# Optimization experiments

Hardware: AMD Instinct MI355X
Metric: run time of the kernel (lower is better)

Reference implementation:

```python
import jax, jax.numpy as jnp
import numpy as np
import math

B, T, D, SLOTS, TOPK = 8, 4096, 512, 128, 8


def setup_inputs() -> dict:
    key = jax.random.key(0)
    kq, kK, kV = jax.random.split(key, 3)
    # xavier_uniform for [slots, d_model]: bound = sqrt(6/(slots+d_model))
    bound = math.sqrt(6.0 / (SLOTS + D))
    return {
        "q": jax.random.normal(kq, (B, T, D), dtype=jnp.float32),
        "K": jax.random.uniform(kK, (SLOTS, D), minval=-bound, maxval=bound, dtype=jnp.float32),
        "V": jax.random.uniform(kV, (SLOTS, D), minval=-bound, maxval=bound, dtype=jnp.float32),
        "salience": jnp.zeros((SLOTS,), dtype=jnp.float32),
        "topk": TOPK,
    }


def reference(q, K, V, salience, topk):
    # q: [B,T,D], K/V: [S,D], salience: [S]
    Bq, Tq, Dq = q.shape
    k = min(topk, K.shape[0])
    scores = jnp.einsum('btd,sd->bts', q, K) / jnp.sqrt(jnp.float32(Dq))
    scores = scores + salience[None, None, :]
    topk_scores, topk_indices = jax.lax.top_k(scores, k)          # [B,T,k]
    attention_weights = jax.nn.softmax(topk_scores, axis=-1)      # [B,T,k]
    V_selected = V[topk_indices]                                  # [B,T,k,D] gather
    read_vectors = jnp.einsum('btk,btkd->btd', attention_weights, V_selected)
    return read_vectors, attention_weights
```

## Files before the change

kernel.cpp:

```cpp
#include <hip/hip_runtime.h>
#include <hip/hip_bf16.h>
#include <math.h>

#define R_TOTAL 32768
#define DM      512
#define NSLOT   128
#define KSEL    8

typedef _Float16 half8 __attribute__((ext_vector_type(8)));
typedef float    floatx4 __attribute__((ext_vector_type(4)));

__global__ void smb_prepK(const float* __restrict__ Km, _Float16* __restrict__ Ks) {
  const int i = blockIdx.x * 256 + threadIdx.x;
  const int slot = i >> 9;
  const int d    = i & 511;
  const float f  = Km[i] * 256.0f;
  const _Float16 h  = (_Float16)f;
  const _Float16 lo = (_Float16)(f - (float)h);
  const int c  = d >> 5;
  const int kg = (d >> 3) & 3;
  const int j  = d & 7;
  Ks[((((c * 8) + kg    ) * NSLOT + slot) << 3) + j] = h;
  Ks[((((c * 8) + 4 + kg) * NSLOT + slot) << 3) + j] = lo;
}

__device__ __forceinline__ void load16_lds(const _Float16* g, _Float16* l) {
  __builtin_amdgcn_global_load_lds(
      (const __attribute__((address_space(1))) unsigned int*)g,
      (__attribute__((address_space(3))) unsigned int*)l, 16, 0, 0);
}

__global__ __launch_bounds__(512, 8) void smb_main(
    const float* __restrict__ q,
    const _Float16* __restrict__ Ks,
    const float* __restrict__ Vm,
    const float* __restrict__ sal,
    float* __restrict__ outv,
    float* __restrict__ outw)
{
  __shared__ union U {
    _Float16 stage[2][8][NSLOT][8];
    float    slab[64][132];
  } u;

  const int t  = threadIdx.x;
  const int w  = t >> 6;
  const int l  = t & 63;
  const int li = l & 15;
  const int kg = l >> 4;
  const int rg = w >> 1;
  const int sh = w & 1;
  const int r0b = blockIdx.x * 64;
  const int r0w = r0b + rg * 16;

  const float* qrow = q + (size_t)(r0w + li) * DM + kg * 8;

  floatx4 acc[4];
#pragma unroll
  for (int g = 0; g < 4; ++g) acc[g] = (floatx4){0.f, 0.f, 0.f, 0.f};

#pragma unroll
  for (int p = 0; p < 2; ++p) {
    const _Float16* src = Ks + ((((size_t)0 * 8 + w) * NSLOT + p * 64 + l) << 3);
    load16_lds(src, &u.stage[0][w][p * 64 + l][0]);
  }
  float4 q0c = *(const float4*)(qrow + 0);
  float4 q1c = *(const float4*)(qrow + 4);
  float4 q0n = *(const float4*)(qrow + 32);
  float4 q1n = *(const float4*)(qrow + 36);
  __syncthreads();

#pragma unroll 2
  for (int c = 0; c < 16; ++c) {
    const int cb = c & 1, nb = cb ^ 1;
    float4 q0nn, q1nn;
    if (c < 15) {
#pragma unroll
      for (int p = 0; p < 2; ++p) {
        const _Float16* src = Ks + ((((size_t)(c + 1) * 8 + w) * NSLOT + p * 64 + l) << 3);
        load16_lds(src, &u.stage[nb][w][p * 64 + l][0]);
      }
    }
    if (c < 14) {
      q0nn = *(const float4*)(qrow + (c + 2) * 32);
      q1nn = *(const float4*)(qrow + (c + 2) * 32 + 4);
    }

    half8 a1, a2;
#pragma unroll
    for (int j = 0; j < 4; ++j) {
      const float f0 = q0c[j] * 16.0f;
      const float f1 = q1c[j] * 16.0f;
      const _Float16 h0 = (_Float16)f0;
      const _Float16 h1 = (_Float16)f1;
      a1[j]     = h0;  a2[j]     = (_Float16)(f0 - (float)h0);
      a1[4 + j] = h1;  a2[4 + j] = (_Float16)(f1 - (float)h1);
    }
#pragma unroll
    for (int g = 0; g < 4; ++g) {
      const int slot = sh * 64 + g * 16 + li;
      const half8 b1 = *(const half8*)&u.stage[cb][kg][slot][0];
      const half8 b2 = *(const half8*)&u.stage[cb][4 + kg][slot][0];
      acc[g] = __builtin_amdgcn_mfma_f32_16x16x32_f16(a1, b1, acc[g], 0, 0, 0);
      acc[g] = __builtin_amdgcn_mfma_f32_16x16x32_f16(a2, b1, acc[g], 0, 0, 0);
      acc[g] = __builtin_amdgcn_mfma_f32_16x16x32_f16(a1, b2, acc[g], 0, 0, 0);
    }
    q0c = q0n; q1c = q1n;
    if (c < 14) { q0n = q0nn; q1n = q1nn; }
    __syncthreads();
  }

  const float den = sqrtf((float)DM);
#pragma unroll
  for (int g = 0; g < 4; ++g) {
    const int col = sh * 64 + g * 16 + li;
    const float sv = sal[col];
#pragma unroll
    for (int i = 0; i < 4; ++i) {
      const float s = (acc[g][i] * 0.000244140625f) / den + sv;
      u.slab[rg * 16 + kg * 4 + i][col] = s;
    }
  }
  __syncthreads();

  const int row = t >> 3;
  const int lq  = t & 7;

  float bs[8]; int bi[8];
#pragma unroll
  for (int p = 0; p < 8; ++p) { bs[p] = -3.0e38f; bi[p] = 0x7fffffff; }

#pragma unroll
  for (int jj = 0; jj < 16; ++jj) {
    const int   j = jj * 8 + lq;
    const float s = u.slab[row][j];
    bool c[8];
#pragma unroll
    for (int p = 0; p < 8; ++p) c[p] = s > bs[p];
    float nb[8]; int ni[8];
    nb[0] = c[0] ? s : bs[0];
    ni[0] = c[0] ? j : bi[0];
#pragma unroll
    for (int p = 7; p >= 1; --p) {
      nb[p] = c[p] ? (c[p - 1] ? bs[p - 1] : s) : bs[p];
      ni[p] = c[p] ? (c[p - 1] ? bi[p - 1] : j) : bi[p];
    }
#pragma unroll
    for (int p = 0; p < 8; ++p) { bs[p] = nb[p]; bi[p] = ni[p]; }
  }

  float ts[8]; int ti_[8];
#pragma unroll
  for (int r = 0; r < 8; ++r) {
    float hs = bs[0]; int hi = bi[0];
#pragma unroll
    for (int m = 1; m <= 4; m <<= 1) {
      const float os = __shfl_xor(hs, m, 64);
      const int   oi = __shfl_xor(hi, m, 64);
      if (os > hs || (os == hs && oi < hi)) { hs = os; hi = oi; }
    }
    ts[r] = hs; ti_[r] = hi;
    if (bs[0] == hs && bi[0] == hi) {
#pragma unroll
      for (int p = 0; p < 7; ++p) { bs[p] = bs[p + 1]; bi[p] = bi[p + 1]; }
      bs[7] = -3.0e38f; bi[7] = 0x7fffffff;
    }
  }

  float tw[8];
  const float mx = ts[0];
  float esum = 0.0f;
#pragma unroll
  for (int r = 0; r < 8; ++r) { tw[r] = expf(ts[r] - mx); esum += tw[r]; }
#pragma unroll
  for (int r = 0; r < 8; ++r) tw[r] /= esum;

  if (lq == 0) {
#pragma unroll
    for (int r = 0; r < 8; ++r) outw[(size_t)(r0b + row) * KSEL + r] = tw[r];
  }

  const float4* __restrict__ V4 = (const float4*)Vm;
  float4* __restrict__ O4 = (float4*)outv;
  const size_t obase = (size_t)(r0b + row) * (DM / 4);
#pragma unroll 4
  for (int cc = 0; cc < 16; ++cc) {
    const int cdx = cc * 8 + lq;
    float4 a; a.x = a.y = a.z = a.w = 0.0f;
#pragma unroll
    for (int r = 0; r < 8; ++r) {
      const float4 v = V4[(size_t)ti_[r] * (DM / 4) + cdx];
      a.x = fmaf(tw[r], v.x, a.x);
      a.y = fmaf(tw[r], v.y, a.y);
      a.z = fmaf(tw[r], v.z, a.z);
      a.w = fmaf(tw[r], v.w, a.w);
    }
    O4[obase + cdx] = a;
  }
}

extern "C" void kernel_launch(void* const* d_in, const int* in_sizes, int n_in,
                              void* d_out, int out_size, void* d_ws, size_t ws_size,
                              hipStream_t stream) {
  const float* q   = (const float*)d_in[0];
  const float* Km  = (const float*)d_in[1];
  const float* Vm  = (const float*)d_in[2];
  const float* sal = (const float*)d_in[3];

  float* outv = (float*)d_out;
  float* outw = outv + (size_t)R_TOTAL * DM;

  _Float16* Ks = (_Float16*)d_ws;

  hipLaunchKernelGGL(smb_prepK, dim3((NSLOT * DM) / 256), dim3(256), 0, stream, Km, Ks);
  hipLaunchKernelGGL(smb_main, dim3(R_TOTAL / 64), dim3(512), 0, stream,
                     q, Ks, Vm, sal, outv, outw);
}
```

Baseline: 68.59 us.

## Double K-chunk width per pipeline stage and vectorize top-k slab reads

The GEMM loop now processes two 32-wide K chunks per iteration (8 iterations instead of 16), staging twice as much of K in LDS per stage. This halves the number of barriers and prefetch rounds. The top-k scan now gives each thread a contiguous 16-element segment read with float4 LDS loads instead of strided scalar reads, and occupancy hint drops from 8 to 4 blocks per CU. The larger LDS stage (32KB union) may reduce occupancy.

After: 68.11 us. No clear change (-0.7%).

```diff
diff --git a/kernel.cpp b/kernel.cpp
--- a/kernel.cpp
+++ b/kernel.cpp
@@ -30,7 +30,7 @@
       (__attribute__((address_space(3))) unsigned int*)l, 16, 0, 0);
 }
 
-__global__ __launch_bounds__(512, 8) void smb_main(
+__global__ __launch_bounds__(512, 4) void smb_main(
     const float* __restrict__ q,
     const _Float16* __restrict__ Ks,
     const float* __restrict__ Vm,
@@ -39,7 +39,7 @@
     float* __restrict__ outw)
 {
   __shared__ union U {
-    _Float16 stage[2][8][NSLOT][8];
+    _Float16 stage[2][2][8][NSLOT][8];
     float    slab[64][132];
   } u;
 
@@ -60,53 +60,60 @@
   for (int g = 0; g < 4; ++g) acc[g] = (floatx4){0.f, 0.f, 0.f, 0.f};
 
 #pragma unroll
-  for (int p = 0; p < 2; ++p) {
-    const _Float16* src = Ks + ((((size_t)0 * 8 + w) * NSLOT + p * 64 + l) << 3);
-    load16_lds(src, &u.stage[0][w][p * 64 + l][0]);
-  }
-  float4 q0c = *(const float4*)(qrow + 0);
-  float4 q1c = *(const float4*)(qrow + 4);
-  float4 q0n = *(const float4*)(qrow + 32);
-  float4 q1n = *(const float4*)(qrow + 36);
+  for (int i = 0; i < 4; ++i) {
+    const int sub = i >> 1, p = i & 1;
+    const _Float16* src = Ks + ((((size_t)(0 + sub) * 8 + w) * NSLOT + p * 64 + l) << 3);
+    load16_lds(src, &u.stage[0][sub][w][p * 64 + l][0]);
+  }
+  float4 qc0 = *(const float4*)(qrow + 0);
+  float4 qc1 = *(const float4*)(qrow + 4);
+  float4 qc2 = *(const float4*)(qrow + 32);
+  float4 qc3 = *(const float4*)(qrow + 36);
   __syncthreads();
 
 #pragma unroll 2
-  for (int c = 0; c < 16; ++c) {
+  for (int c = 0; c < 8; ++c) {
     const int cb = c & 1, nb = cb ^ 1;
-    float4 q0nn, q1nn;
-    if (c < 15) {
-#pragma unroll
-      for (int p = 0; p < 2; ++p) {
-        const _Float16* src = Ks + ((((size_t)(c + 1) * 8 + w) * NSLOT + p * 64 + l) << 3);
-        load16_lds(src, &u.stage[nb][w][p * 64 + l][0]);
-      }
-    }
-    if (c < 14) {
-      q0nn = *(const float4*)(qrow + (c + 2) * 32);
-      q1nn = *(const float4*)(qrow + (c + 2) * 32 + 4);
-    }
-
-    half8 a1, a2;
-#pragma unroll
-    for (int j = 0; j < 4; ++j) {
-      const float f0 = q0c[j] * 16.0f;
-      const float f1 = q1c[j] * 16.0f;
-      const _Float16 h0 = (_Float16)f0;
-      const _Float16 h1 = (_Float16)f1;
-      a1[j]     = h0;  a2[j]     = (_Float16)(f0 - (float)h0);
-      a1[4 + j] = h1;  a2[4 + j] = (_Float16)(f1 - (float)h1);
-    }
-#pragma unroll
-    for (int g = 0; g < 4; ++g) {
-      const int slot = sh * 64 + g * 16 + li;
-      const half8 b1 = *(const half8*)&u.stage[cb][kg][slot][0];
-      const half8 b2 = *(const half8*)&u.stage[cb][4 + kg][slot][0];
-      acc[g] = __builtin_amdgcn_mfma_f32_16x16x32_f16(a1, b1, acc[g], 0, 0, 0);
-      acc[g] = __builtin_amdgcn_mfma_f32_16x16x32_f16(a2, b1, acc[g], 0, 0, 0);
-      acc[g] = __builtin_amdgcn_mfma_f32_16x16x32_f16(a1, b2, acc[g], 0, 0, 0);
-    }
-    q0c = q0n; q1c = q1n;
-    if (c < 14) { q0n = q0nn; q1n = q1nn; }
+    float4 qn0, qn1, qn2, qn3;
+    if (c < 7) {
+#pragma unroll
+      for (int i = 0; i < 4; ++i) {
+        const int sub = i >> 1, p = i & 1;
+        const _Float16* src =
+            Ks + ((((size_t)(2 * (c + 1) + sub) * 8 + w) * NSLOT + p * 64 + l) << 3);
+        load16_lds(src, &u.stage[nb][sub][w][p * 64 + l][0]);
+      }
+      qn0 = *(const float4*)(qrow + (c + 1) * 64);
+      qn1 = *(const float4*)(qrow + (c + 1) * 64 + 4);
+      qn2 = *(const float4*)(qrow + (c + 1) * 64 + 32);
+      qn3 = *(const float4*)(qrow + (c + 1) * 64 + 36);
+    }
+
+#pragma unroll
+    for (int sub = 0; sub < 2; ++sub) {
+      const float4 qa = sub ? qc2 : qc0;
+      const float4 qb = sub ? qc3 : qc1;
+      half8 a1, a2;
+#pragma unroll
+      for (int j = 0; j < 4; ++j) {
+        const float f0 = qa[j] * 16.0f;
+        const float f1 = qb[j] * 16.0f;
+        const _Float16 h0 = (_Float16)f0;
+        const _Float16 h1 = (_Float16)f1;
+        a1[j]     = h0;  a2[j]     = (_Float16)(f0 - (float)h0);
+        a1[4 + j] = h1;  a2[4 + j] = (_Float16)(f1 - (float)h1);
+      }
+#pragma unroll
+      for (int g = 0; g < 4; ++g) {
+        const int slot = sh * 64 + g * 16 + li;
+        const half8 b1 = *(const half8*)&u.stage[cb][sub][kg][slot][0];
+        const half8 b2 = *(const half8*)&u.stage[cb][sub][4 + kg][slot][0];
+        acc[g] = __builtin_amdgcn_mfma_f32_16x16x32_f16(a1, b1, acc[g], 0, 0, 0);
+        acc[g] = __builtin_amdgcn_mfma_f32_16x16x32_f16(a2, b1, acc[g], 0, 0, 0);
+        acc[g] = __builtin_amdgcn_mfma_f32_16x16x32_f16(a1, b2, acc[g], 0, 0, 0);
+      }
+    }
+    qc0 = qn0; qc1 = qn1; qc2 = qn2; qc3 = qn3;
     __syncthreads();
   }
 
@@ -131,22 +138,26 @@
   for (int p = 0; p < 8; ++p) { bs[p] = -3.0e38f; bi[p] = 0x7fffffff; }
 
 #pragma unroll
-  for (int jj = 0; jj < 16; ++jj) {
-    const int   j = jj * 8 + lq;
-    const float s = u.slab[row][j];
-    bool c[8];
-#pragma unroll
-    for (int p = 0; p < 8; ++p) c[p] = s > bs[p];
-    float nb[8]; int ni[8];
-    nb[0] = c[0] ? s : bs[0];
-    ni[0] = c[0] ? j : bi[0];
-#pragma unroll
-    for (int p = 7; p >= 1; --p) {
-      nb[p] = c[p] ? (c[p - 1] ? bs[p - 1] : s) : bs[p];
-      ni[p] = c[p] ? (c[p - 1] ? bi[p - 1] : j) : bi[p];
-    }
-#pragma unroll
-    for (int p = 0; p < 8; ++p) { bs[p] = nb[p]; bi[p] = ni[p]; }
+  for (int e4 = 0; e4 < 4; ++e4) {
+    const float4 v = *(const float4*)&u.slab[row][lq * 16 + e4 * 4];
+#pragma unroll
+    for (int ei = 0; ei < 4; ++ei) {
+      const int   j = lq * 16 + e4 * 4 + ei;
+      const float s = (ei == 0) ? v.x : (ei == 1) ? v.y : (ei == 2) ? v.z : v.w;
+      bool c[8];
+#pragma unroll
+      for (int p = 0; p < 8; ++p) c[p] = s > bs[p];
+      float nb_[8]; int ni[8];
+      nb_[0] = c[0] ? s : bs[0];
+      ni[0]  = c[0] ? j : bi[0];
+#pragma unroll
+      for (int p = 7; p >= 1; --p) {
+        nb_[p] = c[p] ? (c[p - 1] ? bs[p - 1] : s) : bs[p];
+        ni[p]  = c[p] ? (c[p - 1] ? bi[p - 1] : j) : bi[p];
+      }
+#pragma unroll
+      for (int p = 0; p < 8; ++p) { bs[p] = nb_[p]; bi[p] = ni[p]; }
+    }
   }
 
   float ts[8]; int ti_[8];
```

## Compute top-k value gather as sparse-weight MFMA against fp16 transposed V

Applied to the files above, without the earlier changes.

Replaces the per-row scattered gather of eight fp32 V rows with a dense matmul. It builds a 64x128 sparse weight matrix in LDS, split into hi and lo fp16 halves, and multiplies it by an fp16 transposed, swizzled copy of V streamed through LDS with double-buffered async loads. The prep kernel now also writes this V copy. The aim is to cut the scattered global and L2 traffic of the gather epilogue. In exchange V is rounded to fp16, which costs accuracy, and the kernel adds barriers, LDS zeroing and LDS use, so launch bounds are lowered to 4 waves per SIMD.

Result: faster. 57.20 us (-16.6%).

```diff
diff --git a/kernel.cpp b/kernel.cpp
--- a/kernel.cpp
+++ b/kernel.cpp
@@ -10,18 +10,28 @@
 typedef _Float16 half8 __attribute__((ext_vector_type(8)));
 typedef float    floatx4 __attribute__((ext_vector_type(4)));
 
-__global__ void smb_prepK(const float* __restrict__ Km, _Float16* __restrict__ Ks) {
+__global__ void smb_prep(const float* __restrict__ Km, const float* __restrict__ Vm,
+                         _Float16* __restrict__ Ks, _Float16* __restrict__ Vt) {
   const int i = blockIdx.x * 256 + threadIdx.x;
-  const int slot = i >> 9;
-  const int d    = i & 511;
-  const float f  = Km[i] * 256.0f;
-  const _Float16 h  = (_Float16)f;
-  const _Float16 lo = (_Float16)(f - (float)h);
-  const int c  = d >> 5;
-  const int kg = (d >> 3) & 3;
-  const int j  = d & 7;
-  Ks[((((c * 8) + kg    ) * NSLOT + slot) << 3) + j] = h;
-  Ks[((((c * 8) + 4 + kg) * NSLOT + slot) << 3) + j] = lo;
+  {
+    const int slot = i >> 9;
+    const int d    = i & 511;
+    const float f  = Km[i] * 256.0f;
+    const _Float16 h  = (_Float16)f;
+    const _Float16 lo = (_Float16)(f - (float)h);
+    const int c  = d >> 5;
+    const int kg = (d >> 3) & 3;
+    const int j  = d & 7;
+    Ks[((((c * 8) + kg    ) * NSLOT + slot) << 3) + j] = h;
+    Ks[((((c * 8) + 4 + kg) * NSLOT + slot) << 3) + j] = lo;
+  }
+  {
+    const int d    = i >> 7;
+    const int slot = i & 127;
+    const float v  = Vm[(size_t)slot * DM + d];
+    const int idx  = (d >> 6) * 8192 + (d & 63) * 128 + (slot ^ ((d & 7) << 3));
+    Vt[idx] = (_Float16)v;
+  }
 }
 
 __device__ __forceinline__ void load16_lds(const _Float16* g, _Float16* l) {
@@ -30,18 +40,22 @@
       (__attribute__((address_space(3))) unsigned int*)l, 16, 0, 0);
 }
 
-__global__ __launch_bounds__(512, 8) void smb_main(
+__global__ __launch_bounds__(512, 4) void smb_main(
     const float* __restrict__ q,
     const _Float16* __restrict__ Ks,
-    const float* __restrict__ Vm,
+    const _Float16* __restrict__ Vt,
     const float* __restrict__ sal,
     float* __restrict__ outv,
     float* __restrict__ outw)
 {
-  __shared__ union U {
+  __shared__ union R1 {
     _Float16 stage[2][8][NSLOT][8];
+    _Float16 W[2][64][136];
+  } r1;
+  __shared__ union R2 {
     float    slab[64][132];
-  } u;
+    _Float16 vt[2][8192];
+  } r2;
 
   const int t  = threadIdx.x;
   const int w  = t >> 6;
@@ -62,7 +76,7 @@
 #pragma unroll
   for (int p = 0; p < 2; ++p) {
     const _Float16* src = Ks + ((((size_t)0 * 8 + w) * NSLOT + p * 64 + l) << 3);
-    load16_lds(src, &u.stage[0][w][p * 64 + l][0]);
+    load16_lds(src, &r1.stage[0][w][p * 64 + l][0]);
   }
   float4 q0c = *(const float4*)(qrow + 0);
   float4 q1c = *(const float4*)(qrow + 4);
@@ -78,14 +92,13 @@
 #pragma unroll
       for (int p = 0; p < 2; ++p) {
         const _Float16* src = Ks + ((((size_t)(c + 1) * 8 + w) * NSLOT + p * 64 + l) << 3);
-        load16_lds(src, &u.stage[nb][w][p * 64 + l][0]);
+        load16_lds(src, &r1.stage[nb][w][p * 64 + l][0]);
       }
     }
     if (c < 14) {
       q0nn = *(const float4*)(qrow + (c + 2) * 32);
       q1nn = *(const float4*)(qrow + (c + 2) * 32 + 4);
     }
-
     half8 a1, a2;
 #pragma unroll
     for (int j = 0; j < 4; ++j) {
@@ -99,8 +112,8 @@
 #pragma unroll
     for (int g = 0; g < 4; ++g) {
       const int slot = sh * 64 + g * 16 + li;
-      const half8 b1 = *(const half8*)&u.stage[cb][kg][slot][0];
-      const half8 b2 = *(const half8*)&u.stage[cb][4 + kg][slot][0];
+      const half8 b1 = *(const half8*)&r1.stage[cb][kg][slot][0];
+      const half8 b2 = *(const half8*)&r1.stage[cb][4 + kg][slot][0];
       acc[g] = __builtin_amdgcn_mfma_f32_16x16x32_f16(a1, b1, acc[g], 0, 0, 0);
       acc[g] = __builtin_amdgcn_mfma_f32_16x16x32_f16(a2, b1, acc[g], 0, 0, 0);
       acc[g] = __builtin_amdgcn_mfma_f32_16x16x32_f16(a1, b2, acc[g], 0, 0, 0);
@@ -118,7 +131,16 @@
 #pragma unroll
     for (int i = 0; i < 4; ++i) {
       const float s = (acc[g][i] * 0.000244140625f) / den + sv;
-      u.slab[rg * 16 + kg * 4 + i][col] = s;
+      r2.slab[rg * 16 + kg * 4 + i][col] = s;
+    }
+  }
+  {
+    uint4* wz = (uint4*)&r1;
+    const uint4 z4 = {0u, 0u, 0u, 0u};
+#pragma unroll
+    for (int z = 0; z < 5; ++z) {
+      const int idx = t + z * 512;
+      if (idx < 2176) wz[idx] = z4;
     }
   }
   __syncthreads();
@@ -133,20 +155,20 @@
 #pragma unroll
   for (int jj = 0; jj < 16; ++jj) {
     const int   j = jj * 8 + lq;
-    const float s = u.slab[row][j];
+    const float s = r2.slab[row][j];
     bool c[8];
 #pragma unroll
     for (int p = 0; p < 8; ++p) c[p] = s > bs[p];
-    float nb[8]; int ni[8];
-    nb[0] = c[0] ? s : bs[0];
-    ni[0] = c[0] ? j : bi[0];
+    float nb_[8]; int ni[8];
+    nb_[0] = c[0] ? s : bs[0];
+    ni[0]  = c[0] ? j : bi[0];
 #pragma unroll
     for (int p = 7; p >= 1; --p) {
-      nb[p] = c[p] ? (c[p - 1] ? bs[p - 1] : s) : bs[p];
-      ni[p] = c[p] ? (c[p - 1] ? bi[p - 1] : j) : bi[p];
-    }
-#pragma unroll
-    for (int p = 0; p < 8; ++p) { bs[p] = nb[p]; bi[p] = ni[p]; }
+      nb_[p] = c[p] ? (c[p - 1] ? bs[p - 1] : s) : bs[p];
+      ni[p]  = c[p] ? (c[p - 1] ? bi[p - 1] : j) : bi[p];
+    }
+#pragma unroll
+    for (int p = 0; p < 8; ++p) { bs[p] = nb_[p]; bi[p] = ni[p]; }
   }
 
   float ts[8]; int ti_[8];
@@ -180,22 +202,62 @@
     for (int r = 0; r < 8; ++r) outw[(size_t)(r0b + row) * KSEL + r] = tw[r];
   }
 
-  const float4* __restrict__ V4 = (const float4*)Vm;
-  float4* __restrict__ O4 = (float4*)outv;
-  const size_t obase = (size_t)(r0b + row) * (DM / 4);
-#pragma unroll 4
-  for (int cc = 0; cc < 16; ++cc) {
-    const int cdx = cc * 8 + lq;
-    float4 a; a.x = a.y = a.z = a.w = 0.0f;
-#pragma unroll
-    for (int r = 0; r < 8; ++r) {
-      const float4 v = V4[(size_t)ti_[r] * (DM / 4) + cdx];
-      a.x = fmaf(tw[r], v.x, a.x);
-      a.y = fmaf(tw[r], v.y, a.y);
-      a.z = fmaf(tw[r], v.z, a.z);
-      a.w = fmaf(tw[r], v.w, a.w);
-    }
-    O4[obase + cdx] = a;
+  {
+    float wv = tw[0]; int iv = ti_[0];
+#pragma unroll
+    for (int r = 1; r < 8; ++r) { if (lq == r) { wv = tw[r]; iv = ti_[r]; } }
+    const _Float16 wh = (_Float16)wv;
+    const _Float16 wl = (_Float16)(wv - (float)wh);
+    r1.W[0][row][iv] = wh;
+    r1.W[1][row][iv] = wl;
+  }
+  __syncthreads();
+
+  half8 ah[4], al[4];
+#pragma unroll
+  for (int ks = 0; ks < 4; ++ks) {
+    ah[ks] = *(const half8*)&r1.W[0][rg * 16 + li][ks * 32 + kg * 8];
+    al[ks] = *(const half8*)&r1.W[1][rg * 16 + li][ks * 32 + kg * 8];
+  }
+#pragma unroll
+  for (int p = 0; p < 2; ++p) {
+    const _Float16* src = Vt + (size_t)0 * 8192 + w * 1024 + p * 512 + l * 8;
+    load16_lds(src, &r2.vt[0][w * 1024 + p * 512 + l * 8]);
+  }
+  __syncthreads();
+
+  const int swz = (li & 7) << 4;
+#pragma unroll 2
+  for (int cc = 0; cc < 8; ++cc) {
+    const int cb = cc & 1, nb = cb ^ 1;
+    if (cc < 7) {
+#pragma unroll
+      for (int p = 0; p < 2; ++p) {
+        const _Float16* src = Vt + (size_t)(cc + 1) * 8192 + w * 1024 + p * 512 + l * 8;
+        load16_lds(src, &r2.vt[nb][w * 1024 + p * 512 + l * 8]);
+      }
+    }
+    floatx4 acc2[2];
+#pragma unroll
+    for (int nt = 0; nt < 2; ++nt) acc2[nt] = (floatx4){0.f, 0.f, 0.f, 0.f};
+#pragma unroll
+    for (int ks = 0; ks < 4; ++ks) {
+#pragma unroll
+      for (int nt = 0; nt < 2; ++nt) {
+        const int dl  = sh * 32 + nt * 16 + li;
+        const int ofs = (dl * 256 + ks * 64 + kg * 16) ^ swz;
+        const half8 bv = *(const half8*)((const char*)&r2.vt[cb][0] + ofs);
+        acc2[nt] = __builtin_amdgcn_mfma_f32_16x16x32_f16(ah[ks], bv, acc2[nt], 0, 0, 0);
+        acc2[nt] = __builtin_amdgcn_mfma_f32_16x16x32_f16(al[ks], bv, acc2[nt], 0, 0, 0);
+      }
+    }
+#pragma unroll
+    for (int nt = 0; nt < 2; ++nt)
+#pragma unroll
+      for (int i = 0; i < 4; ++i)
+        outv[(size_t)(r0b + rg * 16 + kg * 4 + i) * DM + cc * 64 + sh * 32 + nt * 16 + li]
+            = acc2[nt][i];
+    __syncthreads();
   }
 }
 
@@ -211,8 +273,9 @@
   float* outw = outv + (size_t)R_TOTAL * DM;
 
   _Float16* Ks = (_Float16*)d_ws;
-
-  hipLaunchKernelGGL(smb_prepK, dim3((NSLOT * DM) / 256), dim3(256), 0, stream, Km, Ks);
+  _Float16* Vt = Ks + (size_t)16 * 8 * NSLOT * 8;
+
+  hipLaunchKernelGGL(smb_prep, dim3((NSLOT * DM) / 256), dim3(256), 0, stream, Km, Vm, Ks, Vt);
   hipLaunchKernelGGL(smb_main, dim3(R_TOTAL / 64), dim3(512), 0, stream,
-                     q, Ks, Vm, sal, outv, outw);
-}
+                     q, Ks, Vt, sal, outv, outw);
+}
```

## Double rows per block so each staged K chunk feeds two MFMA row tiles

Applied to the files above, without the earlier changes.

Each block now handles 128 rows instead of 64. Every wave computes two 16-row MFMA tiles against the same LDS-staged K chunk, which halves K staging traffic and barrier count per row. Top-k and the V gather now use 4 threads per row instead of 8, with a shorter shuffle reduction. The cost is more registers per thread (launch bounds relaxed to 2), half as many blocks (256 on the device), and a larger score slab in shared memory, which may reduce occupancy and latency hiding.

Measured after the change: 71.02 us. 3.6% more time.

```diff
diff --git a/kernel.cpp b/kernel.cpp
--- a/kernel.cpp
+++ b/kernel.cpp
@@ -30,7 +30,7 @@
       (__attribute__((address_space(3))) unsigned int*)l, 16, 0, 0);
 }
 
-__global__ __launch_bounds__(512, 8) void smb_main(
+__global__ __launch_bounds__(512, 2) void smb_main(
     const float* __restrict__ q,
     const _Float16* __restrict__ Ks,
     const float* __restrict__ Vm,
@@ -40,7 +40,7 @@
 {
   __shared__ union U {
     _Float16 stage[2][8][NSLOT][8];
-    float    slab[64][132];
+    float    slab[128][132];
   } u;
 
   const int t  = threadIdx.x;
@@ -50,30 +50,34 @@
   const int kg = l >> 4;
   const int rg = w >> 1;
   const int sh = w & 1;
-  const int r0b = blockIdx.x * 64;
-  const int r0w = r0b + rg * 16;
-
-  const float* qrow = q + (size_t)(r0w + li) * DM + kg * 8;
-
-  floatx4 acc[4];
-#pragma unroll
-  for (int g = 0; g < 4; ++g) acc[g] = (floatx4){0.f, 0.f, 0.f, 0.f};
+  const int r0b = blockIdx.x * 128;
+  const int r0w = r0b + rg * 32;
+
+  const float* qrow0 = q + (size_t)(r0w + li) * DM + kg * 8;
+  const float* qrow1 = qrow0 + (size_t)16 * DM;
+
+  floatx4 acc[2][4];
+#pragma unroll
+  for (int rs = 0; rs < 2; ++rs)
+#pragma unroll
+    for (int g = 0; g < 4; ++g) acc[rs][g] = (floatx4){0.f, 0.f, 0.f, 0.f};
 
 #pragma unroll
   for (int p = 0; p < 2; ++p) {
     const _Float16* src = Ks + ((((size_t)0 * 8 + w) * NSLOT + p * 64 + l) << 3);
     load16_lds(src, &u.stage[0][w][p * 64 + l][0]);
   }
-  float4 q0c = *(const float4*)(qrow + 0);
-  float4 q1c = *(const float4*)(qrow + 4);
-  float4 q0n = *(const float4*)(qrow + 32);
-  float4 q1n = *(const float4*)(qrow + 36);
+  float4 qc[4], qn[4];
+  qc[0] = *(const float4*)(qrow0 + 0);  qc[1] = *(const float4*)(qrow0 + 4);
+  qc[2] = *(const float4*)(qrow1 + 0);  qc[3] = *(const float4*)(qrow1 + 4);
+  qn[0] = *(const float4*)(qrow0 + 32); qn[1] = *(const float4*)(qrow0 + 36);
+  qn[2] = *(const float4*)(qrow1 + 32); qn[3] = *(const float4*)(qrow1 + 36);
   __syncthreads();
 
 #pragma unroll 2
   for (int c = 0; c < 16; ++c) {
     const int cb = c & 1, nb = cb ^ 1;
-    float4 q0nn, q1nn;
+    float4 qnn[4];
     if (c < 15) {
 #pragma unroll
       for (int p = 0; p < 2; ++p) {
@@ -82,71 +86,88 @@
       }
     }
     if (c < 14) {
-      q0nn = *(const float4*)(qrow + (c + 2) * 32);
-      q1nn = *(const float4*)(qrow + (c + 2) * 32 + 4);
-    }
-
-    half8 a1, a2;
-#pragma unroll
-    for (int j = 0; j < 4; ++j) {
-      const float f0 = q0c[j] * 16.0f;
-      const float f1 = q1c[j] * 16.0f;
-      const _Float16 h0 = (_Float16)f0;
-      const _Float16 h1 = (_Float16)f1;
-      a1[j]     = h0;  a2[j]     = (_Float16)(f0 - (float)h0);
-      a1[4 + j] = h1;  a2[4 + j] = (_Float16)(f1 - (float)h1);
+      qnn[0] = *(const float4*)(qrow0 + (c + 2) * 32);
+      qnn[1] = *(const float4*)(qrow0 + (c + 2) * 32 + 4);
+      qnn[2] = *(const float4*)(qrow1 + (c + 2) * 32);
+      qnn[3] = *(const float4*)(qrow1 + (c + 2) * 32 + 4);
+    }
+
+    half8 a1[2], a2[2];
+#pragma unroll
+    for (int rs = 0; rs < 2; ++rs) {
+      const float4 qa = qc[rs * 2 + 0];
+      const float4 qb = qc[rs * 2 + 1];
+#pragma unroll
+      for (int j = 0; j < 4; ++j) {
+        const float f0 = qa[j] * 16.0f;
+        const float f1 = qb[j] * 16.0f;
+        const _Float16 h0 = (_Float16)f0;
+        const _Float16 h1 = (_Float16)f1;
+        a1[rs][j]     = h0;  a2[rs][j]     = (_Float16)(f0 - (float)h0);
+        a1[rs][4 + j] = h1;  a2[rs][4 + j] = (_Float16)(f1 - (float)h1);
+      }
     }
 #pragma unroll
     for (int g = 0; g < 4; ++g) {
       const int slot = sh * 64 + g * 16 + li;
       const half8 b1 = *(const half8*)&u.stage[cb][kg][slot][0];
       const half8 b2 = *(const half8*)&u.stage[cb][4 + kg][slot][0];
-      acc[g] = __builtin_amdgcn_mfma_f32_16x16x32_f16(a1, b1, acc[g], 0, 0, 0);
-      acc[g] = __builtin_amdgcn_mfma_f32_16x16x32_f16(a2, b1, acc[g], 0, 0, 0);
-      acc[g] = __builtin_amdgcn_mfma_f32_16x16x32_f16(a1, b2, acc[g], 0, 0, 0);
-    }
-    q0c = q0n; q1c = q1n;
-    if (c < 14) { q0n = q0nn; q1n = q1nn; }
+#pragma unroll
+      for (int rs = 0; rs < 2; ++rs) {
+        acc[rs][g] = __builtin_amdgcn_mfma_f32_16x16x32_f16(a1[rs], b1, acc[rs][g], 0, 0, 0);
+        acc[rs][g] = __builtin_amdgcn_mfma_f32_16x16x32_f16(a2[rs], b1, acc[rs][g], 0, 0, 0);
+        acc[rs][g] = __builtin_amdgcn_mfma_f32_16x16x32_f16(a1[rs], b2, acc[rs][g], 0, 0, 0);
+      }
+    }
+#pragma unroll
+    for (int i = 0; i < 4; ++i) qc[i] = qn[i];
+    if (c < 14) {
+#pragma unroll
+      for (int i = 0; i < 4; ++i) qn[i] = qnn[i];
+    }
     __syncthreads();
   }
 
   const float den = sqrtf((float)DM);
 #pragma unroll
-  for (int g = 0; g < 4; ++g) {
-    const int col = sh * 64 + g * 16 + li;
-    const float sv = sal[col];
-#pragma unroll
-    for (int i = 0; i < 4; ++i) {
-      const float s = (acc[g][i] * 0.000244140625f) / den + sv;
-      u.slab[rg * 16 + kg * 4 + i][col] = s;
+  for (int rs = 0; rs < 2; ++rs) {
+#pragma unroll
+    for (int g = 0; g < 4; ++g) {
+      const int col = sh * 64 + g * 16 + li;
+      const float sv = sal[col];
+#pragma unroll
+      for (int i = 0; i < 4; ++i) {
+        const float s = (acc[rs][g][i] * 0.000244140625f) / den + sv;
+        u.slab[rg * 32 + rs * 16 + kg * 4 + i][col] = s;
+      }
     }
   }
   __syncthreads();
 
-  const int row = t >> 3;
-  const int lq  = t & 7;
+  const int row = t >> 2;
+  const int lq  = t & 3;
 
   float bs[8]; int bi[8];
 #pragma unroll
   for (int p = 0; p < 8; ++p) { bs[p] = -3.0e38f; bi[p] = 0x7fffffff; }
 
 #pragma unroll
-  for (int jj = 0; jj < 16; ++jj) {
-    const int   j = jj * 8 + lq;
+  for (int jj = 0; jj < 32; ++jj) {
+    const int   j = jj * 4 + lq;
     const float s = u.slab[row][j];
     bool c[8];
 #pragma unroll
     for (int p = 0; p < 8; ++p) c[p] = s > bs[p];
-    float nb[8]; int ni[8];
-    nb[0] = c[0] ? s : bs[0];
-    ni[0] = c[0] ? j : bi[0];
+    float nb_[8]; int ni[8];
+    nb_[0] = c[0] ? s : bs[0];
+    ni[0]  = c[0] ? j : bi[0];
 #pragma unroll
     for (int p = 7; p >= 1; --p) {
-      nb[p] = c[p] ? (c[p - 1] ? bs[p - 1] : s) : bs[p];
-      ni[p] = c[p] ? (c[p - 1] ? bi[p - 1] : j) : bi[p];
-    }
-#pragma unroll
-    for (int p = 0; p < 8; ++p) { bs[p] = nb[p]; bi[p] = ni[p]; }
+      nb_[p] = c[p] ? (c[p - 1] ? bs[p - 1] : s) : bs[p];
+      ni[p]  = c[p] ? (c[p - 1] ? bi[p - 1] : j) : bi[p];
+    }
+#pragma unroll
+    for (int p = 0; p < 8; ++p) { bs[p] = nb_[p]; bi[p] = ni[p]; }
   }
 
   float ts[8]; int ti_[8];
@@ -154,7 +175,7 @@
   for (int r = 0; r < 8; ++r) {
     float hs = bs[0]; int hi = bi[0];
 #pragma unroll
-    for (int m = 1; m <= 4; m <<= 1) {
+    for (int m = 1; m <= 2; m <<= 1) {
       const float os = __shfl_xor(hs, m, 64);
       const int   oi = __shfl_xor(hi, m, 64);
       if (os > hs || (os == hs && oi < hi)) { hs = os; hi = oi; }
@@ -184,8 +205,8 @@
   float4* __restrict__ O4 = (float4*)outv;
   const size_t obase = (size_t)(r0b + row) * (DM / 4);
 #pragma unroll 4
-  for (int cc = 0; cc < 16; ++cc) {
-    const int cdx = cc * 8 + lq;
+  for (int cc = 0; cc < 32; ++cc) {
+    const int cdx = cc * 4 + lq;
     float4 a; a.x = a.y = a.z = a.w = 0.0f;
 #pragma unroll
     for (int r = 0; r < 8; ++r) {
@@ -213,6 +234,6 @@
   _Float16* Ks = (_Float16*)d_ws;
 
   hipLaunchKernelGGL(smb_prepK, dim3((NSLOT * DM) / 256), dim3(256), 0, stream, Km, Ks);
-  hipLaunchKernelGGL(smb_main, dim3(R_TOTAL / 64), dim3(512), 0, stream,
+  hipLaunchKernelGGL(smb_main, dim3(R_TOTAL / 128), dim3(512), 0, stream,
                      q, Ks, Vm, sal, outv, outw);
 }
```
